# Kernel tuning notes

Hardware: AMD Instinct MI355X
Metric: run time of the kernel (lower is better)

Reference implementation:

```python
import jax, jax.numpy as jnp
import numpy as np

B, C, T, V = 16, 128, 294, 25
DEPTH = 2
HEADS, DHEAD = 8, 64
INNER = HEADS * DHEAD  # 512
P = 7      # local attention patch size (constructor passes global_k=7 here)
K = 7      # global attention kv stride (constructor passes local_patch_size=7 here)
MULT = 4
SCALE = DHEAD ** -0.5
EPS = 1e-5


def setup_inputs() -> dict:
    key = jax.random.key(0)
    ks = jax.random.split(key, 16)
    d = DEPTH

    def rn(k, shape, s=0.02):
        return jax.random.normal(k, shape, dtype=jnp.float32) * s

    return {
        "x": jax.random.normal(ks[0], (B, C, T, V), dtype=jnp.float32),
        "ln1_g": jnp.ones((d, C), jnp.float32), "ln1_b": jnp.zeros((d, C), jnp.float32),
        "la_wq": rn(ks[1], (d, C, INNER)), "la_wkv": rn(ks[2], (d, C, 2 * INNER)),
        "la_wo": rn(ks[3], (d, INNER, C)), "la_bo": jnp.zeros((d, C), jnp.float32),
        "ln2_g": jnp.ones((d, C), jnp.float32), "ln2_b": jnp.zeros((d, C), jnp.float32),
        "ff1_w1": rn(ks[4], (d, C, MULT * C)), "ff1_b1": jnp.zeros((d, MULT * C), jnp.float32),
        "ff1_w2": rn(ks[5], (d, MULT * C, C)), "ff1_b2": jnp.zeros((d, C), jnp.float32),
        "ln3_g": jnp.ones((d, C), jnp.float32), "ln3_b": jnp.zeros((d, C), jnp.float32),
        "ga_wq": rn(ks[6], (d, C, INNER)), "ga_wkv": rn(ks[7], (d, C, K, 2 * INNER)),
        "ga_wo": rn(ks[8], (d, INNER, C)), "ga_bo": jnp.zeros((d, C), jnp.float32),
        "ln4_g": jnp.ones((d, C), jnp.float32), "ln4_b": jnp.zeros((d, C), jnp.float32),
        "ff2_w1": rn(ks[9], (d, C, MULT * C)), "ff2_b1": jnp.zeros((d, MULT * C), jnp.float32),
        "ff2_w2": rn(ks[10], (d, MULT * C, C)), "ff2_b2": jnp.zeros((d, C), jnp.float32),
    }


def channel_ln(x, g, b):
    # LayerNorm over channel dim (axis=1), biased variance
    m = jnp.mean(x, axis=1, keepdims=True)
    v = jnp.var(x, axis=1, keepdims=True)
    return (x - m) / jnp.sqrt(v + EPS) * g[None, :, None, None] + b[None, :, None, None]


def local_attn(x, wq, wkv, wo, bo):
    b, c, t, v = x.shape
    nt = t // P
    # 'b c (t p) v -> b t v p c'
    f = x.reshape(b, c, nt, P, v).transpose(0, 2, 4, 3, 1)
    q = jnp.einsum('btvpc,ci->btvpi', f, wq).reshape(b, nt, v, P, HEADS, DHEAD)
    kv = jnp.einsum('btvpc,ci->btvpi', f, wkv)
    kk, vv = jnp.split(kv, 2, axis=-1)
    kk = kk.reshape(b, nt, v, P, HEADS, DHEAD)
    vv = vv.reshape(b, nt, v, P, HEADS, DHEAD)
    dots = jnp.einsum('btvihd,btvjhd->btvhij', q, kk) * SCALE  # [b,nt,v,h,P,P]
    attn = jax.nn.softmax(dots, axis=-1)
    out = jnp.einsum('btvhij,btvjhd->btvihd', attn, vv)  # [b,nt,v,P,h,d]
    out = out.transpose(0, 4, 5, 1, 3, 2).reshape(b, INNER, t, v)  # b (h d) (t p) v
    return jnp.einsum('bitv,ic->bctv', out, wo) + bo[None, :, None, None]


def global_attn(x, wq, wkv, wo, bo):
    b, c, t, v = x.shape
    tk = t // K
    q = jnp.einsum('bctv,ci->bitv', x, wq).reshape(b, HEADS, DHEAD, t, v)
    xk = x.reshape(b, c, tk, K, v)  # strided (K,1) conv == blocked contraction
    kv = jnp.einsum('bctkv,cki->bitv', xk, wkv)  # [b, 2*INNER, tk, v]
    kk, vv = jnp.split(kv, 2, axis=1)
    kk = kk.reshape(b, HEADS, DHEAD, tk, v)
    vv = vv.reshape(b, HEADS, DHEAD, tk, v)
    dots = jnp.einsum('bhdiv,bhdjv->bhvij', q, kk) * SCALE  # [b,h,v,t,tk]
    attn = jax.nn.softmax(dots, axis=-1)
    out = jnp.einsum('bhvij,bhdjv->bhdiv', attn, vv).reshape(b, INNER, t, v)
    return jnp.einsum('bitv,ic->bctv', out, wo) + bo[None, :, None, None]


def ff(x, w1, b1, w2, b2):
    h = jax.nn.gelu(jnp.einsum('bctv,ch->bhtv', x, w1) + b1[None, :, None, None],
                    approximate=False)
    return jnp.einsum('bhtv,hc->bctv', h, w2) + b2[None, :, None, None]


def reference(x, ln1_g, ln1_b, la_wq, la_wkv, la_wo, la_bo,
              ln2_g, ln2_b, ff1_w1, ff1_b1, ff1_w2, ff1_b2,
              ln3_g, ln3_b, ga_wq, ga_wkv, ga_wo, ga_bo,
              ln4_g, ln4_b, ff2_w1, ff2_b1, ff2_w2, ff2_b2):
    for i in range(DEPTH):
        x = local_attn(channel_ln(x, ln1_g[i], ln1_b[i]), la_wq[i], la_wkv[i], la_wo[i], la_bo[i]) + x
        x = ff(channel_ln(x, ln2_g[i], ln2_b[i]), ff1_w1[i], ff1_b1[i], ff1_w2[i], ff1_b2[i]) + x
        x = global_attn(channel_ln(x, ln3_g[i], ln3_b[i]), ga_wq[i], ga_wkv[i], ga_wo[i], ga_bo[i]) + x
        x = ff(channel_ln(x, ln4_g[i], ln4_b[i]), ff2_w1[i], ff2_b1[i], ff2_w2[i], ff2_b2[i]) + x
    return x
```

## Files before the change

kernel.cpp:

```cpp
#include <hip/hip_runtime.h>
#include <hip/hip_bf16.h>
#include <math.h>

namespace {

constexpr int Bb   = 16;
constexpr int Cc   = 128;
constexpr int Tt   = 294;
constexpr int Vv   = 25;
constexpr int TV   = Tt * Vv;
constexpr int NPOS = Bb * TV;
constexpr int INNER = 512;
constexpr int HID   = 512;
constexpr int NH    = 8;
constexpr int DH    = 64;
constexpr int Pp    = 7;
constexpr int Kk    = 7;
constexpr int NT    = 42;
constexpr int TK    = 42;
constexpr int NKV   = Bb * TK * Vv;
constexpr float EPS   = 1e-5f;
constexpr float SCALE = 0.125f;

typedef __attribute__((ext_vector_type(8))) short bf16x8;
typedef __attribute__((ext_vector_type(4))) float f32x4;

__device__ inline float bflo(uint32_t u) { union { float f; uint32_t i; } x; x.i = u << 16; return x.f; }
__device__ inline float bfhi(uint32_t u) { union { float f; uint32_t i; } x; x.i = u & 0xffff0000u; return x.f; }
__device__ inline unsigned short f2bf(float f) {
  union { float f; uint32_t i; } x; x.f = f;
  uint32_t r = x.i + 0x7fffu + ((x.i >> 16) & 1u);
  return (unsigned short)(r >> 16);
}

constexpr int OFF_FF1W1 = 0;
constexpr int OFF_FF1W2 = 65536;
constexpr int OFF_FF2W1 = 131072;
constexpr int OFF_FF2W2 = 196608;
constexpr int OFF_GAWQ  = 262144;
constexpr int OFF_GAWO  = 327680;
constexpr int OFF_GAWKV = 393216;
constexpr int OFF_LAWQ  = 1310720;
constexpr int OFF_LAWKV = 1376256;
constexpr int OFF_LAWO  = 1507328;
constexpr size_t LPK = 1572864;

__global__ __launch_bounds__(64) void k_pack(const float* __restrict__ src,
                                             unsigned short* __restrict__ dst,
                                             int nks, int rowStride,
                                             size_t srcLayerStride, size_t dstLayerStride,
                                             int kkSrcOff, int kkDstOff) {
  int bid = blockIdx.x;
  int nt = bid / nks, ks = bid % nks;
  int l = threadIdx.x;
  const float* s = src + (size_t)blockIdx.z * srcLayerStride + (size_t)blockIdx.y * kkSrcOff;
  unsigned short* d = dst + (size_t)blockIdx.z * dstLayerStride + (size_t)blockIdx.y * kkDstOff
                      + ((size_t)bid * 64 + l) * 8;
  int rowb = ks * 32 + (l >> 4) * 8, col = nt * 16 + (l & 15);
  unsigned short tmp[8];
#pragma unroll
  for (int j = 0; j < 8; ++j) tmp[j] = f2bf(s[(size_t)(rowb + j) * rowStride + col]);
#pragma unroll
  for (int j = 0; j < 8; ++j) d[j] = tmp[j];
}

__global__ __launch_bounds__(256) void k_transpose(const float* __restrict__ src,
                                                   float* __restrict__ dst,
                                                   int M, int N) {
  __shared__ float tile[32][33];
  size_t off = (size_t)blockIdx.z * (size_t)M * (size_t)N;
  src += off; dst += off;
  int bx = blockIdx.x * 32, by = blockIdx.y * 32;
  int tx = threadIdx.x, ty = threadIdx.y;
#pragma unroll
  for (int r = 0; r < 4; ++r) {
    int row = by + ty + r * 8, col = bx + tx;
    if (row < M && col < N) tile[ty + r * 8][tx] = src[(size_t)row * N + col];
  }
  __syncthreads();
#pragma unroll
  for (int r = 0; r < 4; ++r) {
    int row = bx + ty + r * 8, col = by + tx;
    if (row < N && col < M) dst[(size_t)row * M + col] = tile[tx][ty + r * 8];
  }
}

__global__ __launch_bounds__(256) void k_stats(const float* __restrict__ xT,
                                               float* __restrict__ mean,
                                               float* __restrict__ rstd) {
  int row  = blockIdx.x * 4 + (threadIdx.x >> 6);
  int lane = threadIdx.x & 63;
  const float* p = xT + (size_t)row * Cc;
  float a = p[lane], b = p[lane + 64];
  float s = a + b, ss = a * a + b * b;
#pragma unroll
  for (int off = 32; off; off >>= 1) {
    s  += __shfl_xor(s, off);
    ss += __shfl_xor(ss, off);
  }
  if (lane == 0) {
    float m = s * (1.0f / Cc);
    mean[row] = m;
    rstd[row] = rsqrtf(ss * (1.0f / Cc) - m * m + EPS);
  }
}

__global__ __launch_bounds__(256) void k_local_mfma(float* __restrict__ xT,
                                                    const float* __restrict__ mean,
                                                    const float* __restrict__ rstd,
                                                    const float* __restrict__ g,
                                                    const float* __restrict__ be,
                                                    const unsigned short* __restrict__ wqpk,
                                                    const unsigned short* __restrict__ wkvpk,
                                                    const unsigned short* __restrict__ wopk,
                                                    const float* __restrict__ bo) {
  constexpr int RR = 49;
  constexpr int QS = 72;
  __shared__ unsigned short xa[64][136];
  __shared__ unsigned short qh[64][QS];
  __shared__ unsigned short kh[64][QS];
  __shared__ unsigned short vh[64][QS];
  __shared__ unsigned short oh[64][QS];
  int bid = blockIdx.x;
  int ch = bid % 6, v = (bid / 6) % Vv, b = bid / (6 * Vv);
  int t0 = ch * RR;
  int tid = threadIdx.x, lane = tid & 63, w = tid >> 6;

  for (int e = tid; e < 64 * 64; e += 256) {
    int r = e >> 6, cp = e & 63;
    uint32_t u = 0;
    if (r < RR) {
      int xrow = (b * Tt + t0 + r) * Vv + v;
      float m = mean[xrow], rs = rstd[xrow];
      const float* xp = xT + (size_t)xrow * Cc + cp * 2;
      float v0 = (xp[0] - m) * rs * g[cp * 2] + be[cp * 2];
      float v1 = (xp[1] - m) * rs * g[cp * 2 + 1] + be[cp * 2 + 1];
      u = (uint32_t)f2bf(v0) | ((uint32_t)f2bf(v1) << 16);
    }
    *(uint32_t*)&xa[r][cp * 2] = u;
  }
  for (int e = tid; e < (64 - RR) * (QS / 2); e += 256) {
    int r = RR + e / (QS / 2), wd = e % (QS / 2);
    *(uint32_t*)&oh[r][wd * 2] = 0;
  }

  f32x4 acc2[8];
#pragma unroll
  for (int n = 0; n < 8; ++n) acc2[n] = (f32x4){0.f, 0.f, 0.f, 0.f};

  for (int h = 0; h < NH; ++h) {
    __syncthreads();
#pragma unroll
    for (int jj = 0; jj < 12; ++jj) {
      int j = w * 12 + jj;
      int mat = j >> 4, mt = (j >> 2) & 3, ntl = j & 3;
      const unsigned short* bp = (mat == 0) ? wqpk : wkvpk;
      int ntg = (mat == 2 ? 32 : 0) + h * 4 + ntl;
      f32x4 a4 = (f32x4){0.f, 0.f, 0.f, 0.f};
#pragma unroll
      for (int ks = 0; ks < 4; ++ks) {
        bf16x8 af = *(const bf16x8*)&xa[mt * 16 + (lane & 15)][ks * 32 + (lane >> 4) * 8];
        bf16x8 bf_ = *(const bf16x8*)&bp[((size_t)(ntg * 4 + ks) * 64 + lane) * 8];
        a4 = __builtin_amdgcn_mfma_f32_16x16x32_bf16(af, bf_, a4, 0, 0, 0);
      }
      unsigned short* dstp = (mat == 0) ? &qh[0][0] : (mat == 1 ? &kh[0][0] : &vh[0][0]);
#pragma unroll
      for (int i = 0; i < 4; ++i)
        dstp[(mt * 16 + (lane >> 4) * 4 + i) * QS + ntl * 16 + (lane & 15)] = f2bf(a4[i]);
    }
    __syncthreads();
    if (tid < 2 * RR) {
      int r = tid >> 1, half = tid & 1;
      int pbase = (r / 7) * 7;
      float q[32];
#pragma unroll
      for (int c = 0; c < 16; ++c) {
        uint32_t u = *(const uint32_t*)&qh[r][half * 32 + c * 2];
        q[2 * c] = bflo(u); q[2 * c + 1] = bfhi(u);
      }
      float s[Pp];
      float mx = -1e30f;
#pragma unroll
      for (int j = 0; j < Pp; ++j) {
        float acc = 0.f;
#pragma unroll
        for (int c = 0; c < 16; ++c) {
          uint32_t u = *(const uint32_t*)&kh[pbase + j][half * 32 + c * 2];
          acc += q[2 * c] * bflo(u) + q[2 * c + 1] * bfhi(u);
        }
        acc += __shfl_xor(acc, 1);
        s[j] = acc * SCALE;
        mx = fmaxf(mx, s[j]);
      }
      float sum = 0.f;
#pragma unroll
      for (int j = 0; j < Pp; ++j) { s[j] = expf(s[j] - mx); sum += s[j]; }
      float inv = 1.0f / sum;
      float o[32];
#pragma unroll
      for (int c = 0; c < 32; ++c) o[c] = 0.f;
#pragma unroll
      for (int j = 0; j < Pp; ++j) {
        float wgt = s[j] * inv;
#pragma unroll
        for (int c = 0; c < 16; ++c) {
          uint32_t u = *(const uint32_t*)&vh[pbase + j][half * 32 + c * 2];
          o[2 * c] += wgt * bflo(u);
          o[2 * c + 1] += wgt * bfhi(u);
        }
      }
#pragma unroll
      for (int c = 0; c < 16; ++c)
        *(uint32_t*)&oh[r][half * 32 + c * 2] =
            (uint32_t)f2bf(o[2 * c]) | ((uint32_t)f2bf(o[2 * c + 1]) << 16);
    }
    __syncthreads();
#pragma unroll
    for (int ksl = 0; ksl < 2; ++ksl) {
      bf16x8 af = *(const bf16x8*)&oh[w * 16 + (lane & 15)][ksl * 32 + (lane >> 4) * 8];
#pragma unroll
      for (int nn = 0; nn < 8; ++nn) {
        bf16x8 bf_ = *(const bf16x8*)&wopk[((size_t)(nn * 16 + h * 2 + ksl) * 64 + lane) * 8];
        acc2[nn] = __builtin_amdgcn_mfma_f32_16x16x32_bf16(af, bf_, acc2[nn], 0, 0, 0);
      }
    }
  }
#pragma unroll
  for (int nn = 0; nn < 8; ++nn) {
    int col = nn * 16 + (lane & 15);
    float bb = bo[col];
#pragma unroll
    for (int i = 0; i < 4; ++i) {
      int r = w * 16 + (lane >> 4) * 4 + i;
      if (r < RR) {
        int row = (b * Tt + t0 + r) * Vv + v;
        xT[(size_t)row * Cc + col] += bb + acc2[nn][i];
      }
    }
  }
}

__global__ __launch_bounds__(256) void k_ff_mfma(float* __restrict__ xT,
                                                 const float* __restrict__ mean,
                                                 const float* __restrict__ rstd,
                                                 const float* __restrict__ g,
                                                 const float* __restrict__ be,
                                                 const unsigned short* __restrict__ w1pk,
                                                 const float* __restrict__ b1,
                                                 const unsigned short* __restrict__ w2pk,
                                                 const float* __restrict__ b2) {
  __shared__ unsigned short xa[32][136];
  __shared__ unsigned short hb[32][520];
  int tid = threadIdx.x, lane = tid & 63, w = tid >> 6;
  int row0 = blockIdx.x * 32;

  for (int e = tid; e < 32 * 64; e += 256) {
    int r = e >> 6, cp = e & 63;
    int row = row0 + r;
    float m = mean[row], rs = rstd[row];
    const float* xp = xT + (size_t)row * Cc + cp * 2;
    float v0 = (xp[0] - m) * rs * g[cp * 2] + be[cp * 2];
    float v1 = (xp[1] - m) * rs * g[cp * 2 + 1] + be[cp * 2 + 1];
    uint32_t u = (uint32_t)f2bf(v0) | ((uint32_t)f2bf(v1) << 16);
    *(uint32_t*)&xa[r][cp * 2] = u;
  }
  __syncthreads();

  f32x4 acc[2][8];
#pragma unroll
  for (int m = 0; m < 2; ++m)
#pragma unroll
    for (int n = 0; n < 8; ++n) acc[m][n] = (f32x4){0.f, 0.f, 0.f, 0.f};
#pragma unroll
  for (int ks = 0; ks < 4; ++ks) {
    bf16x8 a0 = *(const bf16x8*)&xa[(lane & 15)][ks * 32 + (lane >> 4) * 8];
    bf16x8 a1 = *(const bf16x8*)&xa[16 + (lane & 15)][ks * 32 + (lane >> 4) * 8];
#pragma unroll
    for (int nn = 0; nn < 8; ++nn) {
      int ntg = w * 8 + nn;
      bf16x8 bf_ = *(const bf16x8*)&w1pk[((size_t)(ntg * 4 + ks) * 64 + lane) * 8];
      acc[0][nn] = __builtin_amdgcn_mfma_f32_16x16x32_bf16(a0, bf_, acc[0][nn], 0, 0, 0);
      acc[1][nn] = __builtin_amdgcn_mfma_f32_16x16x32_bf16(a1, bf_, acc[1][nn], 0, 0, 0);
    }
  }
#pragma unroll
  for (int m = 0; m < 2; ++m)
#pragma unroll
    for (int nn = 0; nn < 8; ++nn) {
      int col = (w * 8 + nn) * 16 + (lane & 15);
      float bb = b1[col];
#pragma unroll
      for (int i = 0; i < 4; ++i) {
        int r = m * 16 + (lane >> 4) * 4 + i;
        float h = acc[m][nn][i] + bb;
        hb[r][col] = f2bf(0.5f * h * (1.0f + erff(h * 0.70710678118654752f)));
      }
    }
  __syncthreads();

  f32x4 acc2[2][2];
#pragma unroll
  for (int m = 0; m < 2; ++m)
#pragma unroll
    for (int n = 0; n < 2; ++n) acc2[m][n] = (f32x4){0.f, 0.f, 0.f, 0.f};
#pragma unroll
  for (int ks = 0; ks < 16; ++ks) {
    bf16x8 a0 = *(const bf16x8*)&hb[(lane & 15)][ks * 32 + (lane >> 4) * 8];
    bf16x8 a1 = *(const bf16x8*)&hb[16 + (lane & 15)][ks * 32 + (lane >> 4) * 8];
#pragma unroll
    for (int nn = 0; nn < 2; ++nn) {
      int ntg = w * 2 + nn;
      bf16x8 bf_ = *(const bf16x8*)&w2pk[((size_t)(ntg * 16 + ks) * 64 + lane) * 8];
      acc2[0][nn] = __builtin_amdgcn_mfma_f32_16x16x32_bf16(a0, bf_, acc2[0][nn], 0, 0, 0);
      acc2[1][nn] = __builtin_amdgcn_mfma_f32_16x16x32_bf16(a1, bf_, acc2[1][nn], 0, 0, 0);
    }
  }
#pragma unroll
  for (int m = 0; m < 2; ++m)
#pragma unroll
    for (int nn = 0; nn < 2; ++nn) {
      int col = (w * 2 + nn) * 16 + (lane & 15);
      float bb = b2[col];
#pragma unroll
      for (int i = 0; i < 4; ++i) {
        int row = row0 + m * 16 + (lane >> 4) * 4 + i;
        xT[(size_t)row * Cc + col] += bb + acc2[m][nn][i];
      }
    }
}

__global__ __launch_bounds__(256) void k_gkv_mfma(const float* __restrict__ xT,
                                                  const float* __restrict__ mean,
                                                  const float* __restrict__ rstd,
                                                  const float* __restrict__ g,
                                                  const float* __restrict__ be,
                                                  const unsigned short* __restrict__ wkvpk,
                                                  unsigned short* __restrict__ kvg) {
  __shared__ unsigned short xa[32][136];
  int tid = threadIdx.x, lane = tid & 63, w = tid >> 6;
  int g0 = blockIdx.x * 32;
  int nh = blockIdx.y;
  f32x4 acc[2][8];
#pragma unroll
  for (int m = 0; m < 2; ++m)
#pragma unroll
    for (int n = 0; n < 8; ++n) acc[m][n] = (f32x4){0.f, 0.f, 0.f, 0.f};

  for (int kk = 0; kk < 7; ++kk) {
    __syncthreads();
    for (int e = tid; e < 32 * 64; e += 256) {
      int r = e >> 6, cp = e & 63;
      int grow = g0 + r;
      int b = grow / (TK * Vv), rem = grow % (TK * Vv), tk = rem / Vv, v = rem % Vv;
      int xrow = (b * Tt + tk * 7 + kk) * Vv + v;
      float m = mean[xrow], rs = rstd[xrow];
      const float* xp = xT + (size_t)xrow * Cc + cp * 2;
      float v0 = (xp[0] - m) * rs * g[cp * 2] + be[cp * 2];
      float v1 = (xp[1] - m) * rs * g[cp * 2 + 1] + be[cp * 2 + 1];
      *(uint32_t*)&xa[r][cp * 2] = (uint32_t)f2bf(v0) | ((uint32_t)f2bf(v1) << 16);
    }
    __syncthreads();
    const unsigned short* bp = wkvpk + kk * 131072;
#pragma unroll
    for (int ks = 0; ks < 4; ++ks) {
      bf16x8 a0 = *(const bf16x8*)&xa[(lane & 15)][ks * 32 + (lane >> 4) * 8];
      bf16x8 a1 = *(const bf16x8*)&xa[16 + (lane & 15)][ks * 32 + (lane >> 4) * 8];
#pragma unroll
      for (int nn = 0; nn < 8; ++nn) {
        int ntg = nh * 32 + w * 8 + nn;
        bf16x8 bf_ = *(const bf16x8*)&bp[((size_t)(ntg * 4 + ks) * 64 + lane) * 8];
        acc[0][nn] = __builtin_amdgcn_mfma_f32_16x16x32_bf16(a0, bf_, acc[0][nn], 0, 0, 0);
        acc[1][nn] = __builtin_amdgcn_mfma_f32_16x16x32_bf16(a1, bf_, acc[1][nn], 0, 0, 0);
      }
    }
  }
#pragma unroll
  for (int m = 0; m < 2; ++m)
#pragma unroll
    for (int nn = 0; nn < 8; ++nn) {
      int col = nh * 512 + (w * 8 + nn) * 16 + (lane & 15);
#pragma unroll
      for (int i = 0; i < 4; ++i) {
        int grow = g0 + m * 16 + (lane >> 4) * 4 + i;
        kvg[(size_t)grow * 1024 + col] = f2bf(acc[m][nn][i]);
      }
    }
}

__global__ __launch_bounds__(256) void k_gattn3(const float* __restrict__ xT,
                                                const float* __restrict__ mean,
                                                const float* __restrict__ rstd,
                                                const float* __restrict__ g,
                                                const float* __restrict__ be,
                                                const unsigned short* __restrict__ wqpk,
                                                const unsigned short* __restrict__ kvg,
                                                unsigned short* __restrict__ obuf) {
  __shared__ unsigned short xa[112][136];
  __shared__ unsigned short qh[112][66];
  __shared__ unsigned short kh[42][66];
  __shared__ unsigned short vh[42][66];
  int bid = blockIdx.x;
  int ch = bid % 3, v = (bid / 3) % Vv, b = bid / (3 * Vv);
  int t0 = ch * 98;
  int tid = threadIdx.x, lane = tid & 63, w = tid >> 6;

  for (int e = tid; e < 112 * 64; e += 256) {
    int r = e >> 6, cp = e & 63;
    uint32_t u = 0;
    if (r < 98) {
      int xrow = (b * Tt + t0 + r) * Vv + v;
      float m = mean[xrow], rs = rstd[xrow];
      const float* xp = xT + (size_t)xrow * Cc + cp * 2;
      float v0 = (xp[0] - m) * rs * g[cp * 2] + be[cp * 2];
      float v1 = (xp[1] - m) * rs * g[cp * 2 + 1] + be[cp * 2 + 1];
      u = (uint32_t)f2bf(v0) | ((uint32_t)f2bf(v1) << 16);
    }
    *(uint32_t*)&xa[r][cp * 2] = u;
  }

  for (int h = 0; h < NH; ++h) {
    __syncthreads();
#pragma unroll
    for (int jj = 0; jj < 7; ++jj) {
      int j = w * 7 + jj, mt = j >> 2, ntl = j & 3;
      f32x4 a4 = (f32x4){0.f, 0.f, 0.f, 0.f};
#pragma unroll
      for (int ks = 0; ks < 4; ++ks) {
        bf16x8 af = *(const bf16x8*)&xa[mt * 16 + (lane & 15)][ks * 32 + (lane >> 4) * 8];
        bf16x8 bf_ = *(const bf16x8*)&wqpk[((size_t)((h * 4 + ntl) * 4 + ks) * 64 + lane) * 8];
        a4 = __builtin_amdgcn_mfma_f32_16x16x32_bf16(af, bf_, a4, 0, 0, 0);
      }
#pragma unroll
      for (int i = 0; i < 4; ++i)
        qh[mt * 16 + (lane >> 4) * 4 + i][ntl * 16 + (lane & 15)] = f2bf(a4[i]);
    }
    for (int e = tid; e < 42 * 32; e += 256) {
      int j = e >> 5, dw = e & 31;
      const uint32_t* kr = (const uint32_t*)(kvg + ((size_t)(b * TK + j) * Vv + v) * 1024);
      *(uint32_t*)&kh[j][dw * 2] = kr[h * 32 + dw];
      *(uint32_t*)&vh[j][dw * 2] = kr[256 + h * 32 + dw];
    }
    __syncthreads();

    if (tid < 224) {
      int r = tid >> 1, half = tid & 1;
      float q[32];
#pragma unroll
      for (int c = 0; c < 16; ++c) {
        uint32_t u = *(const uint32_t*)&qh[r][half * 32 + c * 2];
        q[2 * c] = bflo(u); q[2 * c + 1] = bfhi(u);
      }
      float s[42];
      float mx = -1e30f;
#pragma unroll 2
      for (int j = 0; j < TK; ++j) {
        float acc = 0.f;
#pragma unroll
        for (int c = 0; c < 16; ++c) {
          uint32_t u = *(const uint32_t*)&kh[j][half * 32 + c * 2];
          acc += q[2 * c] * bflo(u) + q[2 * c + 1] * bfhi(u);
        }
        acc += __shfl_xor(acc, 1);
        s[j] = acc * SCALE;
        mx = fmaxf(mx, s[j]);
      }
      float sum = 0.f;
#pragma unroll
      for (int j = 0; j < TK; ++j) { s[j] = expf(s[j] - mx); sum += s[j]; }
      float inv = 1.0f / sum;
      float o[32];
#pragma unroll
      for (int c = 0; c < 32; ++c) o[c] = 0.f;
#pragma unroll 2
      for (int j = 0; j < TK; ++j) {
        float wgt = s[j] * inv;
#pragma unroll
        for (int c = 0; c < 16; ++c) {
          uint32_t u = *(const uint32_t*)&vh[j][half * 32 + c * 2];
          o[2 * c] += wgt * bflo(u);
          o[2 * c + 1] += wgt * bfhi(u);
        }
      }
      if (r < 98) {
        uint32_t* orow = (uint32_t*)(obuf + ((size_t)(b * Tt + t0 + r) * Vv + v) * 512);
#pragma unroll
        for (int c = 0; c < 16; ++c)
          orow[h * 32 + half * 16 + c] = (uint32_t)f2bf(o[2 * c]) | ((uint32_t)f2bf(o[2 * c + 1]) << 16);
      }
    }
  }
}

__global__ __launch_bounds__(256) void k_proj_mfma(float* __restrict__ xT,
                                                   const unsigned short* __restrict__ A,
                                                   const unsigned short* __restrict__ wpk,
                                                   const float* __restrict__ bo) {
  int tid = threadIdx.x, lane = tid & 63, w = tid >> 6;
  int row0 = blockIdx.x * 32;
  f32x4 acc[2][2];
#pragma unroll
  for (int m = 0; m < 2; ++m)
#pragma unroll
    for (int n = 0; n < 2; ++n) acc[m][n] = (f32x4){0.f, 0.f, 0.f, 0.f};
#pragma unroll 4
  for (int ks = 0; ks < 16; ++ks) {
    bf16x8 a0 = *(const bf16x8*)&A[(size_t)(row0 + (lane & 15)) * 512 + ks * 32 + (lane >> 4) * 8];
    bf16x8 a1 = *(const bf16x8*)&A[(size_t)(row0 + 16 + (lane & 15)) * 512 + ks * 32 + (lane >> 4) * 8];
#pragma unroll
    for (int nn = 0; nn < 2; ++nn) {
      int ntg = w * 2 + nn;
      bf16x8 bf_ = *(const bf16x8*)&wpk[((size_t)(ntg * 16 + ks) * 64 + lane) * 8];
      acc[0][nn] = __builtin_amdgcn_mfma_f32_16x16x32_bf16(a0, bf_, acc[0][nn], 0, 0, 0);
      acc[1][nn] = __builtin_amdgcn_mfma_f32_16x16x32_bf16(a1, bf_, acc[1][nn], 0, 0, 0);
    }
  }
#pragma unroll
  for (int m = 0; m < 2; ++m)
#pragma unroll
    for (int nn = 0; nn < 2; ++nn) {
      int col = (w * 2 + nn) * 16 + (lane & 15);
      float bb = bo[col];
#pragma unroll
      for (int i = 0; i < 4; ++i) {
        int row = row0 + m * 16 + (lane >> 4) * 4 + i;
        xT[(size_t)row * Cc + col] += bb + acc[m][nn][i];
      }
    }
}

}

extern "C" void kernel_launch(void* const* d_in, const int* in_sizes, int n_in,
                              void* d_out, int out_size, void* d_ws, size_t ws_size,
                              hipStream_t stream) {
  const float* x      = (const float*)d_in[0];
  const float* ln1_g  = (const float*)d_in[1];
  const float* ln1_b  = (const float*)d_in[2];
  const float* la_wq  = (const float*)d_in[3];
  const float* la_wkv = (const float*)d_in[4];
  const float* la_wo  = (const float*)d_in[5];
  const float* la_bo  = (const float*)d_in[6];
  const float* ln2_g  = (const float*)d_in[7];
  const float* ln2_b  = (const float*)d_in[8];
  const float* ff1_w1 = (const float*)d_in[9];
  const float* ff1_b1 = (const float*)d_in[10];
  const float* ff1_w2 = (const float*)d_in[11];
  const float* ff1_b2 = (const float*)d_in[12];
  const float* ln3_g  = (const float*)d_in[13];
  const float* ln3_b  = (const float*)d_in[14];
  const float* ga_wq  = (const float*)d_in[15];
  const float* ga_wkv = (const float*)d_in[16];
  const float* ga_wo  = (const float*)d_in[17];
  const float* ga_bo  = (const float*)d_in[18];
  const float* ln4_g  = (const float*)d_in[19];
  const float* ln4_b  = (const float*)d_in[20];
  const float* ff2_w1 = (const float*)d_in[21];
  const float* ff2_b1 = (const float*)d_in[22];
  const float* ff2_w2 = (const float*)d_in[23];
  const float* ff2_b2 = (const float*)d_in[24];

  float* xT   = (float*)d_ws;
  float* mean = xT + (size_t)NPOS * Cc;
  float* rstd = mean + NPOS;
  unsigned short* obuf = (unsigned short*)(rstd + NPOS);
  unsigned short* kvg  = obuf + (size_t)NPOS * 512;
  unsigned short* wpk  = kvg + (size_t)NKV * 1024;

  hipLaunchKernelGGL(k_pack, dim3(32 * 4, 1, 2), dim3(64), 0, stream,
                     ff1_w1, wpk + OFF_FF1W1, 4, 512, (size_t)65536, LPK, 0, 0);
  hipLaunchKernelGGL(k_pack, dim3(8 * 16, 1, 2), dim3(64), 0, stream,
                     ff1_w2, wpk + OFF_FF1W2, 16, 128, (size_t)65536, LPK, 0, 0);
  hipLaunchKernelGGL(k_pack, dim3(32 * 4, 1, 2), dim3(64), 0, stream,
                     ff2_w1, wpk + OFF_FF2W1, 4, 512, (size_t)65536, LPK, 0, 0);
  hipLaunchKernelGGL(k_pack, dim3(8 * 16, 1, 2), dim3(64), 0, stream,
                     ff2_w2, wpk + OFF_FF2W2, 16, 128, (size_t)65536, LPK, 0, 0);
  hipLaunchKernelGGL(k_pack, dim3(32 * 4, 1, 2), dim3(64), 0, stream,
                     ga_wq, wpk + OFF_GAWQ, 4, 512, (size_t)65536, LPK, 0, 0);
  hipLaunchKernelGGL(k_pack, dim3(8 * 16, 1, 2), dim3(64), 0, stream,
                     ga_wo, wpk + OFF_GAWO, 16, 128, (size_t)65536, LPK, 0, 0);
  hipLaunchKernelGGL(k_pack, dim3(64 * 4, 7, 2), dim3(64), 0, stream,
                     ga_wkv, wpk + OFF_GAWKV, 4, 7168, (size_t)917504, LPK, 1024, 131072);
  hipLaunchKernelGGL(k_pack, dim3(32 * 4, 1, 2), dim3(64), 0, stream,
                     la_wq, wpk + OFF_LAWQ, 4, 512, (size_t)65536, LPK, 0, 0);
  hipLaunchKernelGGL(k_pack, dim3(64 * 4, 1, 2), dim3(64), 0, stream,
                     la_wkv, wpk + OFF_LAWKV, 4, 1024, (size_t)131072, LPK, 0, 0);
  hipLaunchKernelGGL(k_pack, dim3(8 * 16, 1, 2), dim3(64), 0, stream,
                     la_wo, wpk + OFF_LAWO, 16, 128, (size_t)65536, LPK, 0, 0);

  dim3 blk2(32, 8);
  hipLaunchKernelGGL(k_transpose, dim3((TV + 31) / 32, (Cc + 31) / 32, Bb), blk2, 0, stream,
                     x, xT, Cc, TV);

  for (int i = 0; i < 2; ++i) {
    const unsigned short* lw = wpk + (size_t)i * LPK;

    hipLaunchKernelGGL(k_stats, dim3(NPOS / 4), dim3(256), 0, stream, xT, mean, rstd);
    hipLaunchKernelGGL(k_local_mfma, dim3(Bb * Vv * 6), dim3(256), 0, stream,
                       xT, mean, rstd, ln1_g + i * Cc, ln1_b + i * Cc,
                       lw + OFF_LAWQ, lw + OFF_LAWKV, lw + OFF_LAWO, la_bo + i * Cc);

    hipLaunchKernelGGL(k_stats, dim3(NPOS / 4), dim3(256), 0, stream, xT, mean, rstd);
    hipLaunchKernelGGL(k_ff_mfma, dim3(NPOS / 32), dim3(256), 0, stream,
                       xT, mean, rstd, ln2_g + i * Cc, ln2_b + i * Cc,
                       lw + OFF_FF1W1, ff1_b1 + i * HID, lw + OFF_FF1W2, ff1_b2 + i * Cc);

    hipLaunchKernelGGL(k_stats, dim3(NPOS / 4), dim3(256), 0, stream, xT, mean, rstd);
    hipLaunchKernelGGL(k_gkv_mfma, dim3(NKV / 32, 2), dim3(256), 0, stream,
                       xT, mean, rstd, ln3_g + i * Cc, ln3_b + i * Cc,
                       lw + OFF_GAWKV, kvg);
    hipLaunchKernelGGL(k_gattn3, dim3(Bb * Vv * 3), dim3(256), 0, stream,
                       xT, mean, rstd, ln3_g + i * Cc, ln3_b + i * Cc,
                       lw + OFF_GAWQ, kvg, obuf);
    hipLaunchKernelGGL(k_proj_mfma, dim3(NPOS / 32), dim3(256), 0, stream,
                       xT, obuf, lw + OFF_GAWO, ga_bo + i * Cc);

    hipLaunchKernelGGL(k_stats, dim3(NPOS / 4), dim3(256), 0, stream, xT, mean, rstd);
    hipLaunchKernelGGL(k_ff_mfma, dim3(NPOS / 32), dim3(256), 0, stream,
                       xT, mean, rstd, ln4_g + i * Cc, ln4_b + i * Cc,
                       lw + OFF_FF2W1, ff2_b1 + i * HID, lw + OFF_FF2W2, ff2_b2 + i * Cc);
  }

  hipLaunchKernelGGL(k_transpose, dim3((Cc + 31) / 32, (TV + 31) / 32, Bb), blk2, 0, stream,
                     xT, (float*)d_out, TV, Cc);
}
```

Measured before the change: 3.470 ms.

## Fuse global attention output projection and use MFMA for QK and PV

Rewrites the global attention kernel so the score and probability-times-V products run on MFMA instructions instead of scalar per-thread dot products. The output projection and residual add are folded into the same kernel, accumulating per head, which removes the separate projection launch and the bf16 intermediate buffer round trip through global memory. Tiles change from 98-row to 64-row chunks (5 per sequence), with padding and masking for the 42-key dimension. Costs are extra LDS traffic (V transpose, probability tile), more syncs per head, and wasted rows in the last chunk.

```diff
diff --git a/kernel.cpp b/kernel.cpp
--- a/kernel.cpp
+++ b/kernel.cpp
@@ -387,27 +387,33 @@
     }
 }
 
-__global__ __launch_bounds__(256) void k_gattn3(const float* __restrict__ xT,
+__global__ __launch_bounds__(256) void k_gattn4(float* __restrict__ xT,
                                                 const float* __restrict__ mean,
                                                 const float* __restrict__ rstd,
                                                 const float* __restrict__ g,
                                                 const float* __restrict__ be,
                                                 const unsigned short* __restrict__ wqpk,
                                                 const unsigned short* __restrict__ kvg,
-                                                unsigned short* __restrict__ obuf) {
-  __shared__ unsigned short xa[112][136];
-  __shared__ unsigned short qh[112][66];
-  __shared__ unsigned short kh[42][66];
-  __shared__ unsigned short vh[42][66];
+                                                const unsigned short* __restrict__ wopk,
+                                                const float* __restrict__ bo) {
+  __shared__ unsigned short xa[64][136];
+  __shared__ unsigned short qh[64][72];
+  __shared__ unsigned short kh[48][72];
+  __shared__ unsigned short vht[64][72];
+  __shared__ unsigned short pq[64][72];
+  __shared__ unsigned short oh[64][72];
+
   int bid = blockIdx.x;
-  int ch = bid % 3, v = (bid / 3) % Vv, b = bid / (3 * Vv);
-  int t0 = ch * 98;
+  int ch = bid % 5, v = (bid / 5) % Vv, b = bid / (5 * Vv);
+  int t0 = ch * 64;
+  int nR = (Tt - t0 < 64) ? (Tt - t0) : 64;
   int tid = threadIdx.x, lane = tid & 63, w = tid >> 6;
-
-  for (int e = tid; e < 112 * 64; e += 256) {
+  int lc = lane & 15, lg = lane >> 4;
+
+  for (int e = tid; e < 64 * 64; e += 256) {
     int r = e >> 6, cp = e & 63;
     uint32_t u = 0;
-    if (r < 98) {
+    if (r < nR) {
       int xrow = (b * Tt + t0 + r) * Vv + v;
       float m = mean[xrow], rs = rstd[xrow];
       const float* xp = xT + (size_t)xrow * Cc + cp * 2;
@@ -417,115 +423,121 @@
     }
     *(uint32_t*)&xa[r][cp * 2] = u;
   }
+  __syncthreads();
+
+  f32x4 acc2[8];
+#pragma unroll
+  for (int n = 0; n < 8; ++n) acc2[n] = (f32x4){0.f, 0.f, 0.f, 0.f};
 
   for (int h = 0; h < NH; ++h) {
-    __syncthreads();
-#pragma unroll
-    for (int jj = 0; jj < 7; ++jj) {
-      int j = w * 7 + jj, mt = j >> 2, ntl = j & 3;
+#pragma unroll
+    for (int ntl = 0; ntl < 4; ++ntl) {
       f32x4 a4 = (f32x4){0.f, 0.f, 0.f, 0.f};
 #pragma unroll
       for (int ks = 0; ks < 4; ++ks) {
-        bf16x8 af = *(const bf16x8*)&xa[mt * 16 + (lane & 15)][ks * 32 + (lane >> 4) * 8];
+        bf16x8 af = *(const bf16x8*)&xa[w * 16 + lc][ks * 32 + lg * 8];
         bf16x8 bf_ = *(const bf16x8*)&wqpk[((size_t)((h * 4 + ntl) * 4 + ks) * 64 + lane) * 8];
         a4 = __builtin_amdgcn_mfma_f32_16x16x32_bf16(af, bf_, a4, 0, 0, 0);
       }
 #pragma unroll
       for (int i = 0; i < 4; ++i)
-        qh[mt * 16 + (lane >> 4) * 4 + i][ntl * 16 + (lane & 15)] = f2bf(a4[i]);
-    }
-    for (int e = tid; e < 42 * 32; e += 256) {
+        qh[w * 16 + lg * 4 + i][ntl * 16 + lc] = f2bf(a4[i]);
+    }
+    for (int e = tid; e < 48 * 32; e += 256) {
       int j = e >> 5, dw = e & 31;
-      const uint32_t* kr = (const uint32_t*)(kvg + ((size_t)(b * TK + j) * Vv + v) * 1024);
-      *(uint32_t*)&kh[j][dw * 2] = kr[h * 32 + dw];
-      *(uint32_t*)&vh[j][dw * 2] = kr[256 + h * 32 + dw];
-    }
-    __syncthreads();
-
-    if (tid < 224) {
-      int r = tid >> 1, half = tid & 1;
-      float q[32];
-#pragma unroll
-      for (int c = 0; c < 16; ++c) {
-        uint32_t u = *(const uint32_t*)&qh[r][half * 32 + c * 2];
-        q[2 * c] = bflo(u); q[2 * c + 1] = bfhi(u);
-      }
-      float s[42];
-      float mx = -1e30f;
-#pragma unroll 2
-      for (int j = 0; j < TK; ++j) {
-        float acc = 0.f;
-#pragma unroll
-        for (int c = 0; c < 16; ++c) {
-          uint32_t u = *(const uint32_t*)&kh[j][half * 32 + c * 2];
-          acc += q[2 * c] * bflo(u) + q[2 * c + 1] * bfhi(u);
-        }
-        acc += __shfl_xor(acc, 1);
-        s[j] = acc * SCALE;
-        mx = fmaxf(mx, s[j]);
-      }
-      float sum = 0.f;
-#pragma unroll
-      for (int j = 0; j < TK; ++j) { s[j] = expf(s[j] - mx); sum += s[j]; }
-      float inv = 1.0f / sum;
-      float o[32];
-#pragma unroll
-      for (int c = 0; c < 32; ++c) o[c] = 0.f;
-#pragma unroll 2
-      for (int j = 0; j < TK; ++j) {
-        float wgt = s[j] * inv;
-#pragma unroll
-        for (int c = 0; c < 16; ++c) {
-          uint32_t u = *(const uint32_t*)&vh[j][half * 32 + c * 2];
-          o[2 * c] += wgt * bflo(u);
-          o[2 * c + 1] += wgt * bfhi(u);
-        }
-      }
-      if (r < 98) {
-        uint32_t* orow = (uint32_t*)(obuf + ((size_t)(b * Tt + t0 + r) * Vv + v) * 512);
-#pragma unroll
-        for (int c = 0; c < 16; ++c)
-          orow[h * 32 + half * 16 + c] = (uint32_t)f2bf(o[2 * c]) | ((uint32_t)f2bf(o[2 * c + 1]) << 16);
-      }
-    }
-  }
-}
-
-__global__ __launch_bounds__(256) void k_proj_mfma(float* __restrict__ xT,
-                                                   const unsigned short* __restrict__ A,
-                                                   const unsigned short* __restrict__ wpk,
-                                                   const float* __restrict__ bo) {
-  int tid = threadIdx.x, lane = tid & 63, w = tid >> 6;
-  int row0 = blockIdx.x * 32;
-  f32x4 acc[2][2];
-#pragma unroll
-  for (int m = 0; m < 2; ++m)
-#pragma unroll
-    for (int n = 0; n < 2; ++n) acc[m][n] = (f32x4){0.f, 0.f, 0.f, 0.f};
-#pragma unroll 4
-  for (int ks = 0; ks < 16; ++ks) {
-    bf16x8 a0 = *(const bf16x8*)&A[(size_t)(row0 + (lane & 15)) * 512 + ks * 32 + (lane >> 4) * 8];
-    bf16x8 a1 = *(const bf16x8*)&A[(size_t)(row0 + 16 + (lane & 15)) * 512 + ks * 32 + (lane >> 4) * 8];
-#pragma unroll
-    for (int nn = 0; nn < 2; ++nn) {
-      int ntg = w * 2 + nn;
-      bf16x8 bf_ = *(const bf16x8*)&wpk[((size_t)(ntg * 16 + ks) * 64 + lane) * 8];
-      acc[0][nn] = __builtin_amdgcn_mfma_f32_16x16x32_bf16(a0, bf_, acc[0][nn], 0, 0, 0);
-      acc[1][nn] = __builtin_amdgcn_mfma_f32_16x16x32_bf16(a1, bf_, acc[1][nn], 0, 0, 0);
-    }
-  }
-#pragma unroll
-  for (int m = 0; m < 2; ++m)
-#pragma unroll
-    for (int nn = 0; nn < 2; ++nn) {
-      int col = (w * 2 + nn) * 16 + (lane & 15);
-      float bb = bo[col];
+      uint32_t u = 0;
+      if (j < TK)
+        u = *(const uint32_t*)(kvg + (((size_t)(b * TK + j) * Vv + v) * 1024 + h * 64 + dw * 2));
+      *(uint32_t*)&kh[j][dw * 2] = u;
+    }
+    for (int e = tid; e < 64 * 32; e += 256) {
+      int j = e >> 5, dp = e & 31;
+      uint32_t u = 0;
+      if (j < TK)
+        u = *(const uint32_t*)(kvg + (((size_t)(b * TK + j) * Vv + v) * 1024 + 512 + h * 64 + dp * 2));
+      vht[dp * 2][j]     = (unsigned short)(u & 0xffffu);
+      vht[dp * 2 + 1][j] = (unsigned short)(u >> 16);
+    }
+    __syncthreads();
+
+    bf16x8 bq0 = *(const bf16x8*)&qh[w * 16 + lc][lg * 8];
+    bf16x8 bq1 = *(const bf16x8*)&qh[w * 16 + lc][32 + lg * 8];
+    f32x4 st[3];
+#pragma unroll
+    for (int t = 0; t < 3; ++t) {
+      st[t] = (f32x4){0.f, 0.f, 0.f, 0.f};
+      bf16x8 ak0 = *(const bf16x8*)&kh[t * 16 + lc][lg * 8];
+      bf16x8 ak1 = *(const bf16x8*)&kh[t * 16 + lc][32 + lg * 8];
+      st[t] = __builtin_amdgcn_mfma_f32_16x16x32_bf16(ak0, bq0, st[t], 0, 0, 0);
+      st[t] = __builtin_amdgcn_mfma_f32_16x16x32_bf16(ak1, bq1, st[t], 0, 0, 0);
+    }
+    float sv[12];
+#pragma unroll
+    for (int t = 0; t < 3; ++t)
 #pragma unroll
       for (int i = 0; i < 4; ++i) {
-        int row = row0 + m * 16 + (lane >> 4) * 4 + i;
-        xT[(size_t)row * Cc + col] += bb + acc[m][nn][i];
-      }
-    }
+        int kv = t * 16 + lg * 4 + i;
+        sv[t * 4 + i] = (kv < TK) ? st[t][i] * SCALE : -1e30f;
+      }
+    float mx = sv[0];
+#pragma unroll
+    for (int k = 1; k < 12; ++k) mx = fmaxf(mx, sv[k]);
+    mx = fmaxf(mx, __shfl_xor(mx, 16));
+    mx = fmaxf(mx, __shfl_xor(mx, 32));
+    float sum = 0.f;
+#pragma unroll
+    for (int k = 0; k < 12; ++k) { sv[k] = expf(sv[k] - mx); sum += sv[k]; }
+    sum += __shfl_xor(sum, 16);
+    sum += __shfl_xor(sum, 32);
+    float inv = 1.0f / sum;
+#pragma unroll
+    for (int t = 0; t < 3; ++t)
+#pragma unroll
+      for (int i = 0; i < 4; ++i)
+        pq[w * 16 + lc][t * 16 + lg * 4 + i] = f2bf(sv[t * 4 + i] * inv);
+#pragma unroll
+    for (int i = 0; i < 4; ++i)
+      pq[w * 16 + lc][48 + lg * 4 + i] = 0;
+    __syncthreads();
+
+    bf16x8 av0 = *(const bf16x8*)&vht[w * 16 + lc][lg * 8];
+    bf16x8 av1 = *(const bf16x8*)&vht[w * 16 + lc][32 + lg * 8];
+#pragma unroll
+    for (int qt = 0; qt < 4; ++qt) {
+      f32x4 ot = (f32x4){0.f, 0.f, 0.f, 0.f};
+      bf16x8 bp0 = *(const bf16x8*)&pq[qt * 16 + lc][lg * 8];
+      bf16x8 bp1 = *(const bf16x8*)&pq[qt * 16 + lc][32 + lg * 8];
+      ot = __builtin_amdgcn_mfma_f32_16x16x32_bf16(av0, bp0, ot, 0, 0, 0);
+      ot = __builtin_amdgcn_mfma_f32_16x16x32_bf16(av1, bp1, ot, 0, 0, 0);
+#pragma unroll
+      for (int i = 0; i < 4; ++i)
+        oh[qt * 16 + lc][w * 16 + lg * 4 + i] = f2bf(ot[i]);
+    }
+    __syncthreads();
+
+#pragma unroll
+    for (int ksl = 0; ksl < 2; ++ksl) {
+      bf16x8 af = *(const bf16x8*)&oh[w * 16 + lc][ksl * 32 + lg * 8];
+#pragma unroll
+      for (int nn = 0; nn < 8; ++nn) {
+        bf16x8 bf_ = *(const bf16x8*)&wopk[((size_t)(nn * 16 + h * 2 + ksl) * 64 + lane) * 8];
+        acc2[nn] = __builtin_amdgcn_mfma_f32_16x16x32_bf16(af, bf_, acc2[nn], 0, 0, 0);
+      }
+    }
+  }
+#pragma unroll
+  for (int nn = 0; nn < 8; ++nn) {
+    int col = nn * 16 + lc;
+    float bb = bo[col];
+#pragma unroll
+    for (int i = 0; i < 4; ++i) {
+      int r = w * 16 + lg * 4 + i;
+      if (r < nR) {
+        int row = (b * Tt + t0 + r) * Vv + v;
+        xT[(size_t)row * Cc + col] += bb + acc2[nn][i];
+      }
+    }
+  }
 }
 
 }
@@ -608,11 +620,9 @@
     hipLaunchKernelGGL(k_gkv_mfma, dim3(NKV / 32, 2), dim3(256), 0, stream,
                        xT, mean, rstd, ln3_g + i * Cc, ln3_b + i * Cc,
                        lw + OFF_GAWKV, kvg);
-    hipLaunchKernelGGL(k_gattn3, dim3(Bb * Vv * 3), dim3(256), 0, stream,
+    hipLaunchKernelGGL(k_gattn4, dim3(Bb * Vv * 5), dim3(256), 0, stream,
                        xT, mean, rstd, ln3_g + i * Cc, ln3_b + i * Cc,
-                       lw + OFF_GAWQ, kvg, obuf);
-    hipLaunchKernelGGL(k_proj_mfma, dim3(NPOS / 32), dim3(256), 0, stream,
-                       xT, obuf, lw + OFF_GAWO, ga_bo + i * Cc);
+                       lw + OFF_GAWQ, kvg, lw + OFF_GAWO, ga_bo + i * Cc);
 
     hipLaunchKernelGGL(k_stats, dim3(NPOS / 4), dim3(256), 0, stream, xT, mean, rstd);
     hipLaunchKernelGGL(k_ff_mfma, dim3(NPOS / 32), dim3(256), 0, stream,
```

Result: faster. 2.777 ms (-20.0%).
